# Performance work log

Measured on AMD Instinct MI355X. Metric: run time of the kernel, lower is better.

The kernel has to match this reference:

```python
import jax, jax.numpy as jnp
import numpy as np

TOP_K = 2


def setup_inputs() -> dict:
    key = jax.random.key(0)
    ks = jax.random.split(key, 4)
    T, E, D_IN, D_H, D_OUT = 8192, 8, 1024, 4096, 1024
    s_in = 1.0 / np.sqrt(D_IN)
    s_h = 1.0 / np.sqrt(D_H)
    return {
        "x": jax.random.normal(ks[0], (T, D_IN), dtype=jnp.float32),
        "Wg": jax.random.normal(ks[1], (D_IN, E), dtype=jnp.float32) * s_in,
        "bg": jnp.zeros((E,), dtype=jnp.float32),
        "W1": jax.random.normal(ks[2], (E, D_IN, D_H), dtype=jnp.float32) * s_in,
        "b1": jnp.zeros((E, D_H), dtype=jnp.float32),
        "W2": jax.random.normal(ks[3], (E, D_H, D_OUT), dtype=jnp.float32) * s_h,
        "b2": jnp.zeros((E, D_OUT), dtype=jnp.float32),
    }


def moe_forward(x, Wg, bg, W1, b1, W2, b2):
    # Top-k gate: logits [T,E] -> top-k -> softmax over the k selected logits,
    # scattered back into a dense [T,E] weight matrix (zeros elsewhere).
    logits = x @ Wg + bg                              # [T, E]
    topv, topi = jax.lax.top_k(logits, TOP_K)         # [T, k]
    topw = jax.nn.softmax(topv, axis=-1)              # [T, k]
    T, E = logits.shape
    weights = jnp.zeros((T, E), dtype=logits.dtype)
    rows = jnp.arange(T)[:, None]
    weights = weights.at[rows, topi].set(topw)        # dense gate weights [T, E]

    # Dense all-expert MLP (faithful to the naive torch module):
    h = jax.nn.relu(jnp.einsum("ti,eih->teh", x, W1) + b1[None])   # [T, E, H]
    expert_out = jnp.einsum("teh,eho->teo", h, W2) + b2[None]      # [T, E, O]

    # Top-k weighted sum over experts.
    return jnp.einsum("te,teo->to", weights, expert_out)           # [T, O]


def reference(x, Wg, bg, W1, b1, W2, b2):
    return moe_forward(x, Wg, bg, W1, b1, W2, b2)
```

## Files before the change

kernel.cpp:

```cpp
#include <hip/hip_runtime.h>
#include <hip/hip_bf16.h>
#include <stdint.h>

#define NTOK 8192
#define NE 8
#define DIN 1024
#define DH 4096
#define DOUT 1024
#define MAXMB 135

typedef __bf16 bf16;
typedef __bf16 bf16_8 __attribute__((ext_vector_type(8)));
typedef __bf16 bf16_4 __attribute__((ext_vector_type(4)));
typedef float f32_4 __attribute__((ext_vector_type(4)));

__device__ __forceinline__ void gl_lds16(const void* g, void* l) {
  __builtin_amdgcn_global_load_lds(
      (const __attribute__((address_space(1))) unsigned int*)g,
      (__attribute__((address_space(3))) unsigned int*)l, 16, 0, 0);
}

__global__ void gate_kernel(const float* __restrict__ x, const float* __restrict__ Wg,
                            const float* __restrict__ bg,
                            int* __restrict__ topi, float* __restrict__ topw) {
  int t = blockIdx.x * 4 + (threadIdx.x >> 6);
  int lane = threadIdx.x & 63;
  float acc[NE];
#pragma unroll
  for (int e = 0; e < NE; e++) acc[e] = 0.f;
  const float* xr = x + (size_t)t * DIN;
#pragma unroll
  for (int i = 0; i < DIN / 64; i++) {
    float xv = xr[lane + 64 * i];
    const float4* wr = (const float4*)(Wg + (size_t)(lane + 64 * i) * NE);
    float4 w0 = wr[0], w1 = wr[1];
    acc[0] += xv * w0.x; acc[1] += xv * w0.y; acc[2] += xv * w0.z; acc[3] += xv * w0.w;
    acc[4] += xv * w1.x; acc[5] += xv * w1.y; acc[6] += xv * w1.z; acc[7] += xv * w1.w;
  }
#pragma unroll
  for (int off = 32; off > 0; off >>= 1)
#pragma unroll
    for (int e = 0; e < NE; e++) acc[e] += __shfl_xor(acc[e], off, 64);
  if (lane == 0) {
    float lg[NE];
#pragma unroll
    for (int e = 0; e < NE; e++) lg[e] = acc[e] + bg[e];
    int i0 = 0; float v0 = lg[0];
#pragma unroll
    for (int e = 1; e < NE; e++) if (lg[e] > v0) { v0 = lg[e]; i0 = e; }
    int i1 = -1; float v1 = -3.0e38f;
#pragma unroll
    for (int e = 0; e < NE; e++) if (e != i0 && lg[e] > v1) { v1 = lg[e]; i1 = e; }
    float ex = expf(v1 - v0);
    float w0 = 1.f / (1.f + ex);
    float w1 = ex / (1.f + ex);
    topi[2 * t] = i0; topi[2 * t + 1] = i1;
    topw[2 * t] = w0; topw[2 * t + 1] = w1;
  }
}

__global__ void hist_kernel(const int* __restrict__ topi, int* __restrict__ counts,
                            int* __restrict__ pos) {
  __shared__ int bins[NE];
  __shared__ int base[NE];
  int tid = threadIdx.x;
  if (tid < NE) bins[tid] = 0;
  __syncthreads();
  int i = blockIdx.x * 256 + tid;
  int e = topi[i];
  int local = atomicAdd(&bins[e], 1);
  __syncthreads();
  if (tid < NE) base[tid] = atomicAdd(&counts[tid], bins[tid]);
  __syncthreads();
  pos[i] = base[e] + local;
}

__global__ void scan_kernel(const int* counts, int* offsets, int* mblk_off) {
  if (threadIdx.x == 0) {
    int s = 0, b = 0;
    for (int e = 0; e < NE; e++) {
      offsets[e] = s; mblk_off[e] = b;
      s += counts[e]; b += (counts[e] + 127) >> 7;
    }
    mblk_off[NE] = b;
  }
}

__global__ void pack_kernel(const int* __restrict__ topi,
                            const int* __restrict__ pos, const int* __restrict__ offsets,
                            int* __restrict__ tok_list, int* __restrict__ slot_of) {
  int i = blockIdx.x * 256 + threadIdx.x;
  int e = topi[i];
  int slot = offsets[e] + pos[i];
  tok_list[slot] = i >> 1;
  slot_of[i] = slot;
}

__global__ void cvtx_kernel(const float* __restrict__ x, bf16* __restrict__ xb) {
  size_t i = ((size_t)blockIdx.x * 256 + threadIdx.x) * 8;
  float4 a = *(const float4*)(x + i);
  float4 b = *(const float4*)(x + i + 4);
  bf16_8 o;
  o[0] = (bf16)a.x; o[1] = (bf16)a.y; o[2] = (bf16)a.z; o[3] = (bf16)a.w;
  o[4] = (bf16)b.x; o[5] = (bf16)b.y; o[6] = (bf16)b.z; o[7] = (bf16)b.w;
  *(bf16_8*)(xb + i) = o;
}

__global__ void tcvt_kernel(const float* __restrict__ src, bf16* __restrict__ dst,
                            int src_ld, long long src_es, int dst_ld, long long dst_es) {
  __shared__ bf16 tile[32][33];
  const float* s = src + blockIdx.z * src_es + (size_t)(blockIdx.x * 32) * src_ld + blockIdx.y * 32;
  bf16* d = dst + blockIdx.z * dst_es + (size_t)(blockIdx.y * 32) * dst_ld + blockIdx.x * 32;
  int tid = threadIdx.x;
  int r = tid >> 3, c4 = (tid & 7) * 4;
  float4 v = *(const float4*)(s + (size_t)r * src_ld + c4);
  tile[r][c4] = (bf16)v.x; tile[r][c4 + 1] = (bf16)v.y;
  tile[r][c4 + 2] = (bf16)v.z; tile[r][c4 + 3] = (bf16)v.w;
  __syncthreads();
  int n = tid >> 3, k4 = (tid & 7) * 4;
  bf16_4 o;
  o[0] = tile[k4][n]; o[1] = tile[k4 + 1][n]; o[2] = tile[k4 + 2][n]; o[3] = tile[k4 + 3][n];
  *(bf16_4*)(d + (size_t)n * dst_ld + k4) = o;
}



#define XCD_SWIZZLE()                                                     \
  int nbx = gridDim.x;                                                    \
  int orig = blockIdx.y * nbx + blockIdx.x;                               \
  int nwg = nbx * gridDim.y;             \
  int wgid = (orig & 7) * (nwg >> 3) + (orig >> 3);                       \
  int bxi = wgid % nbx;                                                   \
  int mb = wgid / nbx;

__global__ __launch_bounds__(256) void gemm1_kernel(
    const bf16* __restrict__ xb, const bf16* __restrict__ W1t,
    const float* __restrict__ b1, const int* __restrict__ counts,
    const int* __restrict__ offsets, const int* __restrict__ mblk_off,
    const int* __restrict__ tok_list,
    bf16* __restrict__ h, int hchunk, int hc0) {
  XCD_SWIZZLE();
  if (mb >= mblk_off[NE]) return;
  int e = 0;
  while (mb >= mblk_off[e + 1]) e++;
  int ne = counts[e];
  int m0 = (mb - mblk_off[e]) * 128;
  int off = offsets[e];
  int n0 = bxi * 128;

  __shared__ bf16 ldsA[3 * 128 * 32];
  __shared__ bf16 ldsB[3 * 128 * 32];

  int tid = threadIdx.x;
  int w = tid >> 6, lane = tid & 63;
  int scol = (((lane & 3) ^ (lane >> 3)) & 3) * 8;

  const bf16* gA[2]; const bf16* gB[2];
  bf16* lA[2]; bf16* lB[2];
#pragma unroll
  for (int j = 0; j < 2; j++) {
    int seg = w * 2 + j;
    int row = seg * 16 + (lane >> 2);
    int slot = off + m0 + row;
    int smax = off + ne - 1;
    if (slot > smax) slot = smax;
    int tok = tok_list[slot];
    gA[j] = xb + (size_t)tok * DIN + scol;
    lA[j] = ldsA + seg * 512;
    gB[j] = W1t + ((size_t)e * hchunk + n0 + row) * DIN + scol;
    lB[j] = ldsB + seg * 512;
  }

  f32_4 acc[4][4];
#pragma unroll
  for (int i = 0; i < 4; i++)
#pragma unroll
    for (int j = 0; j < 4; j++) acc[i][j] = (f32_4){0.f, 0.f, 0.f, 0.f};

  int wm = w & 1, wn = w >> 1;
  int lr = lane & 15, quad = lane >> 4;
  int rcol = ((quad ^ (lr >> 1)) & 3) * 8;

  auto compute = [&](int buf) {
    bf16_8 af[4], bfr[4];
#pragma unroll
    for (int mt = 0; mt < 4; mt++)
      af[mt] = *(const bf16_8*)(ldsA + buf * 4096 + (wm * 64 + mt * 16 + lr) * 32 + rcol);
#pragma unroll
    for (int nt = 0; nt < 4; nt++)
      bfr[nt] = *(const bf16_8*)(ldsB + buf * 4096 + (wn * 64 + nt * 16 + lr) * 32 + rcol);
#pragma unroll
    for (int mt = 0; mt < 4; mt++)
#pragma unroll
      for (int nt = 0; nt < 4; nt++)
        acc[mt][nt] = __builtin_amdgcn_mfma_f32_16x16x32_bf16(af[mt], bfr[nt], acc[mt][nt], 0, 0, 0);
  };

  const int nk = DIN / 32;
#pragma unroll
  for (int j = 0; j < 2; j++) { gl_lds16(gA[j], lA[j]); gl_lds16(gB[j], lB[j]); }
  gA[0] += 32; gA[1] += 32; gB[0] += 32; gB[1] += 32;
#pragma unroll
  for (int j = 0; j < 2; j++) { gl_lds16(gA[j], lA[j] + 4096); gl_lds16(gB[j], lB[j] + 4096); }
  gA[0] += 32; gA[1] += 32; gB[0] += 32; gB[1] += 32;

  int rb = 0, sb = 2;
  for (int kt = 0; kt < nk; kt++) {
    if (kt + 1 < nk) asm volatile("s_waitcnt vmcnt(4)" ::: "memory");
    else             asm volatile("s_waitcnt vmcnt(0)" ::: "memory");
    __builtin_amdgcn_s_barrier();
    compute(rb);
    if (kt + 2 < nk) {
#pragma unroll
      for (int j = 0; j < 2; j++) {
        gl_lds16(gA[j], lA[j] + sb * 4096);
        gl_lds16(gB[j], lB[j] + sb * 4096);
      }
      gA[0] += 32; gA[1] += 32; gB[0] += 32; gB[1] += 32;
    }
    rb = rb == 2 ? 0 : rb + 1;
    sb = sb == 2 ? 0 : sb + 1;
  }

#pragma unroll
  for (int nt = 0; nt < 4; nt++) {
    int cloc = wn * 64 + nt * 16 + lr;
    int c = n0 + cloc;
    float bias = b1[(size_t)e * DH + hc0 + c];
#pragma unroll
    for (int mt = 0; mt < 4; mt++) {
#pragma unroll
      for (int r2 = 0; r2 < 4; r2++) {
        int row = wm * 64 + mt * 16 + quad * 4 + r2;
        if (m0 + row < ne) {
          float v = acc[mt][nt][r2] + bias;
          v = v > 0.f ? v : 0.f;
          h[(size_t)(off + m0 + row) * hchunk + c] = (bf16)v;
        }
      }
    }
  }
}

__global__ __launch_bounds__(256) void gemm2_kernel(
    const bf16* __restrict__ h, const bf16* __restrict__ W2t,
    const int* __restrict__ counts, const int* __restrict__ offsets,
    const int* __restrict__ mblk_off,
    float* __restrict__ y, int hchunk, int accum) {
  XCD_SWIZZLE();
  if (mb >= mblk_off[NE]) return;
  int e = 0;
  while (mb >= mblk_off[e + 1]) e++;
  int ne = counts[e];
  int m0 = (mb - mblk_off[e]) * 128;
  int off = offsets[e];
  int n0 = bxi * 128;

  __shared__ bf16 ldsA[3 * 128 * 32];
  __shared__ bf16 ldsB[3 * 128 * 32];

  int tid = threadIdx.x;
  int w = tid >> 6, lane = tid & 63;
  int scol = (((lane & 3) ^ (lane >> 3)) & 3) * 8;

  const bf16* gA[2]; const bf16* gB[2];
  bf16* lA[2]; bf16* lB[2];
#pragma unroll
  for (int j = 0; j < 2; j++) {
    int seg = w * 2 + j;
    int row = seg * 16 + (lane >> 2);
    gA[j] = h + (size_t)(off + m0 + row) * hchunk + scol;
    lA[j] = ldsA + seg * 512;
    gB[j] = W2t + ((size_t)e * DOUT + n0 + row) * hchunk + scol;
    lB[j] = ldsB + seg * 512;
  }

  f32_4 acc[4][4];
#pragma unroll
  for (int i = 0; i < 4; i++)
#pragma unroll
    for (int j = 0; j < 4; j++) acc[i][j] = (f32_4){0.f, 0.f, 0.f, 0.f};

  int wm = w & 1, wn = w >> 1;
  int lr = lane & 15, quad = lane >> 4;
  int rcol = ((quad ^ (lr >> 1)) & 3) * 8;

  auto compute = [&](int buf) {
    bf16_8 af[4], bfr[4];
#pragma unroll
    for (int mt = 0; mt < 4; mt++)
      af[mt] = *(const bf16_8*)(ldsA + buf * 4096 + (wm * 64 + mt * 16 + lr) * 32 + rcol);
#pragma unroll
    for (int nt = 0; nt < 4; nt++)
      bfr[nt] = *(const bf16_8*)(ldsB + buf * 4096 + (wn * 64 + nt * 16 + lr) * 32 + rcol);
#pragma unroll
    for (int mt = 0; mt < 4; mt++)
#pragma unroll
      for (int nt = 0; nt < 4; nt++)
        acc[mt][nt] = __builtin_amdgcn_mfma_f32_16x16x32_bf16(af[mt], bfr[nt], acc[mt][nt], 0, 0, 0);
  };

  const int nk = hchunk / 32;
#pragma unroll
  for (int j = 0; j < 2; j++) { gl_lds16(gA[j], lA[j]); gl_lds16(gB[j], lB[j]); }
  gA[0] += 32; gA[1] += 32; gB[0] += 32; gB[1] += 32;
#pragma unroll
  for (int j = 0; j < 2; j++) { gl_lds16(gA[j], lA[j] + 4096); gl_lds16(gB[j], lB[j] + 4096); }
  gA[0] += 32; gA[1] += 32; gB[0] += 32; gB[1] += 32;

  int rb = 0, sb = 2;
  for (int kt = 0; kt < nk; kt++) {
    if (kt + 1 < nk) asm volatile("s_waitcnt vmcnt(4)" ::: "memory");
    else             asm volatile("s_waitcnt vmcnt(0)" ::: "memory");
    __builtin_amdgcn_s_barrier();
    compute(rb);
    if (kt + 2 < nk) {
#pragma unroll
      for (int j = 0; j < 2; j++) {
        gl_lds16(gA[j], lA[j] + sb * 4096);
        gl_lds16(gB[j], lB[j] + sb * 4096);
      }
      gA[0] += 32; gA[1] += 32; gB[0] += 32; gB[1] += 32;
    }
    rb = rb == 2 ? 0 : rb + 1;
    sb = sb == 2 ? 0 : sb + 1;
  }

#pragma unroll
  for (int mt = 0; mt < 4; mt++) {
#pragma unroll
    for (int r2 = 0; r2 < 4; r2++) {
      int row = wm * 64 + mt * 16 + quad * 4 + r2;
      if (m0 + row < ne) {
        float* yrow = y + (size_t)(off + m0 + row) * DOUT + n0;
#pragma unroll
        for (int nt = 0; nt < 4; nt++) {
          int c = wn * 64 + nt * 16 + lr;
          float v = acc[mt][nt][r2];
          if (accum) v += yrow[c];
          yrow[c] = v;
        }
      }
    }
  }
}

__global__ void combine_kernel(const int* __restrict__ topi, const float* __restrict__ topw,
                               const int* __restrict__ slot_of, const float* __restrict__ y,
                               const float* __restrict__ b2, float* __restrict__ out) {
  int t = blockIdx.x;
  int c = threadIdx.x * 4;
  int e0 = topi[2 * t], e1 = topi[2 * t + 1];
  float w0 = topw[2 * t], w1 = topw[2 * t + 1];
  int s0 = slot_of[2 * t], s1 = slot_of[2 * t + 1];
  float4 a = *(const float4*)(y + (size_t)s0 * DOUT + c);
  float4 b = *(const float4*)(y + (size_t)s1 * DOUT + c);
  float4 p = *(const float4*)(b2 + (size_t)e0 * DOUT + c);
  float4 q = *(const float4*)(b2 + (size_t)e1 * DOUT + c);
  float4 o;
  o.x = w0 * (a.x + p.x) + w1 * (b.x + q.x);
  o.y = w0 * (a.y + p.y) + w1 * (b.y + q.y);
  o.z = w0 * (a.z + p.z) + w1 * (b.z + q.z);
  o.w = w0 * (a.w + p.w) + w1 * (b.w + q.w);
  *(float4*)(out + (size_t)t * DOUT + c) = o;
}

extern "C" void kernel_launch(void* const* d_in, const int* in_sizes, int n_in,
                              void* d_out, int out_size, void* d_ws, size_t ws_size,
                              hipStream_t stream) {
  const float* x  = (const float*)d_in[0];
  const float* Wg = (const float*)d_in[1];
  const float* bg = (const float*)d_in[2];
  const float* W1 = (const float*)d_in[3];
  const float* b1 = (const float*)d_in[4];
  const float* W2 = (const float*)d_in[5];
  const float* b2 = (const float*)d_in[6];
  float* out = (float*)d_out;

  char* p = (char*)d_ws;
  int*   counts   = (int*)p;   p += 256;
  int*   offsets  = (int*)p;   p += 256;
  int*   mblk_off = (int*)p;   p += 256;
  int*   topi     = (int*)p;   p += 16384 * 4;
  float* topw     = (float*)p; p += 16384 * 4;
  int*   pos      = (int*)p;   p += 16384 * 4;
  int*   tok_list = (int*)p;   p += 16384 * 4;
  int*   slot_of  = (int*)p;   p += 16384 * 4;
  bf16*  xb       = (bf16*)p;  p += (size_t)NTOK * DIN * 2;
  float* y        = (float*)p; p += (size_t)16384 * DOUT * 4;

  size_t fixedBytes = (size_t)(p - (char*)d_ws);
  int hchunk = 4096;
  while (hchunk > 128 && fixedBytes + (size_t)hchunk * 65792 > ws_size) hchunk >>= 1;

  bf16* W1t  = (bf16*)p; p += (size_t)NE * hchunk * DIN * 2;
  bf16* W2t  = (bf16*)p; p += (size_t)NE * DOUT * hchunk * 2;
  bf16* hbuf = (bf16*)p; p += (size_t)(16384 + 128) * hchunk * 2;

  hipMemsetAsync(counts, 0, 32, stream);
  gate_kernel<<<NTOK / 4, 256, 0, stream>>>(x, Wg, bg, topi, topw);
  cvtx_kernel<<<(NTOK * DIN) / (8 * 256), 256, 0, stream>>>(x, xb);
  hist_kernel<<<64, 256, 0, stream>>>(topi, counts, pos);
  scan_kernel<<<1, 64, 0, stream>>>(counts, offsets, mblk_off);
  pack_kernel<<<64, 256, 0, stream>>>(topi, pos, offsets, tok_list, slot_of);

  int nchunks = DH / hchunk;
  for (int c = 0; c < nchunks; c++) {
    int hc0 = c * hchunk;
    tcvt_kernel<<<dim3(DIN / 32, hchunk / 32, NE), 256, 0, stream>>>(
        W1 + hc0, W1t, DH, (long long)DIN * DH, DIN, (long long)hchunk * DIN);
    tcvt_kernel<<<dim3(hchunk / 32, DOUT / 32, NE), 256, 0, stream>>>(
        W2 + (size_t)hc0 * DOUT, W2t, DOUT, (long long)DH * DOUT, hchunk, (long long)DOUT * hchunk);
    gemm1_kernel<<<dim3(hchunk / 128, MAXMB), 256, 0, stream>>>(
        xb, W1t, b1, counts, offsets, mblk_off, tok_list, hbuf, hchunk, hc0);
    gemm2_kernel<<<dim3(DOUT / 128, MAXMB), 256, 0, stream>>>(
        hbuf, W2t, counts, offsets, mblk_off, y, hchunk, c > 0 ? 1 : 0);
  }
  combine_kernel<<<NTOK, 256, 0, stream>>>(topi, topw, slot_of, y, b2, out);
}
```

Baseline: 833.2 us.

## Issue next-tile loads before MFMA compute and stage gemm1 epilogue through LDS

In both grouped GEMM kernels, the global-to-LDS prefetch for tile kt+2 is now issued before the MFMA work on tile kt, with sched_barriers pinning that order, so memory latency overlaps compute earlier. Safety of the 3-buffer ring depends on the barrier at the start of each iteration, since the slot being written was last read in the previous iteration. The gemm1 epilogue now writes the bias+ReLU bf16 results into a swizzled LDS tile and then stores 16-byte vectors row by row to h, replacing scattered 2-byte global stores. This adds two __syncthreads and some LDS traffic in exchange for coalesced writes.

After: 769.7 us. 7.6% less time.

```diff
diff --git a/kernel.cpp b/kernel.cpp
--- a/kernel.cpp
+++ b/kernel.cpp
@@ -148,8 +148,9 @@
   int off = offsets[e];
   int n0 = bxi * 128;
 
-  __shared__ bf16 ldsA[3 * 128 * 32];
-  __shared__ bf16 ldsB[3 * 128 * 32];
+  __shared__ __align__(16) bf16 smem[6 * 128 * 32];
+  bf16* ldsA = smem;
+  bf16* ldsB = smem + 3 * 4096;
 
   int tid = threadIdx.x;
   int w = tid >> 6, lane = tid & 63;
@@ -209,7 +210,7 @@
     if (kt + 1 < nk) asm volatile("s_waitcnt vmcnt(4)" ::: "memory");
     else             asm volatile("s_waitcnt vmcnt(0)" ::: "memory");
     __builtin_amdgcn_s_barrier();
-    compute(rb);
+    __builtin_amdgcn_sched_barrier(0);
     if (kt + 2 < nk) {
 #pragma unroll
       for (int j = 0; j < 2; j++) {
@@ -218,26 +219,38 @@
       }
       gA[0] += 32; gA[1] += 32; gB[0] += 32; gB[1] += 32;
     }
+    __builtin_amdgcn_sched_barrier(0);
+    compute(rb);
     rb = rb == 2 ? 0 : rb + 1;
     sb = sb == 2 ? 0 : sb + 1;
   }
 
+  __syncthreads();
 #pragma unroll
   for (int nt = 0; nt < 4; nt++) {
     int cloc = wn * 64 + nt * 16 + lr;
-    int c = n0 + cloc;
-    float bias = b1[(size_t)e * DH + hc0 + c];
+    float bias = b1[(size_t)e * DH + hc0 + n0 + cloc];
 #pragma unroll
     for (int mt = 0; mt < 4; mt++) {
 #pragma unroll
       for (int r2 = 0; r2 < 4; r2++) {
         int row = wm * 64 + mt * 16 + quad * 4 + r2;
-        if (m0 + row < ne) {
-          float v = acc[mt][nt][r2] + bias;
-          v = v > 0.f ? v : 0.f;
-          h[(size_t)(off + m0 + row) * hchunk + c] = (bf16)v;
-        }
+        float v = acc[mt][nt][r2] + bias;
+        v = v > 0.f ? v : 0.f;
+        int byte = (row * 256 + cloc * 2) ^ (((row >> 2) & 7) << 4);
+        *(bf16*)((char*)smem + byte) = (bf16)v;
       }
+    }
+  }
+  __syncthreads();
+#pragma unroll
+  for (int p = 0; p < 8; p++) {
+    int r = p * 16 + (tid >> 4);
+    int b = tid & 15;
+    if (m0 + r < ne) {
+      int byte = (r * 256 + b * 16) ^ (((r >> 2) & 7) << 4);
+      bf16_8 v = *(const bf16_8*)((char*)smem + byte);
+      *(bf16_8*)(h + (size_t)(off + m0 + r) * hchunk + n0 + b * 8) = v;
     }
   }
 }
@@ -256,8 +269,9 @@
   int off = offsets[e];
   int n0 = bxi * 128;
 
-  __shared__ bf16 ldsA[3 * 128 * 32];
-  __shared__ bf16 ldsB[3 * 128 * 32];
+  __shared__ __align__(16) bf16 smem[6 * 128 * 32];
+  bf16* ldsA = smem;
+  bf16* ldsB = smem + 3 * 4096;
 
   int tid = threadIdx.x;
   int w = tid >> 6, lane = tid & 63;
@@ -313,7 +327,7 @@
     if (kt + 1 < nk) asm volatile("s_waitcnt vmcnt(4)" ::: "memory");
     else             asm volatile("s_waitcnt vmcnt(0)" ::: "memory");
     __builtin_amdgcn_s_barrier();
-    compute(rb);
+    __builtin_amdgcn_sched_barrier(0);
     if (kt + 2 < nk) {
 #pragma unroll
       for (int j = 0; j < 2; j++) {
@@ -322,6 +336,8 @@
       }
       gA[0] += 32; gA[1] += 32; gB[0] += 32; gB[1] += 32;
     }
+    __builtin_amdgcn_sched_barrier(0);
+    compute(rb);
     rb = rb == 2 ? 0 : rb + 1;
     sb = sb == 2 ? 0 : sb + 1;
   }
```
